# Optimization experiments

Hardware: AMD Instinct MI355X
Metric: run time of the kernel (lower is better)

Reference implementation:

```python
import jax, jax.numpy as jnp
import numpy as np

# --- configuration constants (from OpticalDotProductConfiguration) ---
INPUT_BITS = 8
ADC_BITS = 8
DAC_VMIN, DAC_VMAX = 0.0, 1.0
ADC_VMAX = 1.0
OPT_GAIN = 10.0
AWG_XTALK = 0.01
MZM_VMIN, MZM_VMAX = 0.0, 1.0
MZM_LOSS = 10.0 ** (-0.5 / 10.0)   # loss_dB_to_linear(0.5)
YB_LOSS = 10.0 ** (-0.3 / 10.0)
MRR_LOSS = 10.0 ** (-0.5 / 10.0)
MRR_XTALK = 0.01
PD_RESP = 1.0
PD_DARK = 1e-12
PD_R = 50.0
PD_HZ = 10.0 * 1e9
PD_T = 300.0
TIA_GAIN = 100.0
K_B = 1.380649e-23
Q_E = 1.602176634e-19

B, N = 4096, 8192


def conv_same(x, kernel):
    # x: [B, N], kernel: [K]; torch F.conv1d = cross-correlation, same as lax conv
    out = jax.lax.conv_general_dilated(
        x[:, None, :], kernel[None, None, :], (1,), 'SAME')
    return out[:, 0, :]


def setup_inputs() -> dict:
    key = jax.random.key(0)
    ks = jax.random.split(key, 6)
    return {
        'x': jax.random.normal(ks[0], (B, N), dtype=jnp.float32),
        'weights': jax.random.normal(ks[1], (N,), dtype=jnp.float32),
        'noise_tp': jax.random.normal(ks[2], (B,), dtype=jnp.float32),
        'noise_sp': jax.random.normal(ks[3], (B,), dtype=jnp.float32),
        'noise_tn': jax.random.normal(ks[4], (B,), dtype=jnp.float32),
        'noise_sn': jax.random.normal(ks[5], (B,), dtype=jnp.float32),
    }


def reference(x, weights, noise_tp, noise_sp, noise_tn, noise_sn):
    dt = x.dtype
    # software_implemented_transformation
    wnorm = jnp.max(jnp.abs(weights))
    wnorm = jnp.where(wnorm <= 1e-9, jnp.asarray(1.0, dt), wnorm)
    wt = weights / wnorm
    w_abs = jnp.abs(wt)            # weight DAC is identity for weights
    w_pos = wt >= 0                # [N] bool

    t_pos = x > 0                  # [B, N]
    ax = jnp.abs(x)
    inorm = jnp.max(ax, axis=1)
    inorm = jnp.where(inorm <= 1e-9, jnp.asarray(1.0, dt), inorm)[:, None]
    maxq_in = 2 ** INPUT_BITS - 1
    q = jnp.round(ax / inorm * maxq_in)

    # input DAC
    d = jnp.round(jnp.clip(q, 0.0, maxq_in)) / maxq_in
    d = DAC_VMIN + (DAC_VMAX - DAC_VMIN) * d

    # laser: gain + AWG crosstalk conv
    lk = jnp.array([AWG_XTALK / 4, AWG_XTALK, 1.0, AWG_XTALK, AWG_XTALK / 4], dtype=dt)
    l = conv_same(d * OPT_GAIN, lk)

    # MZM
    m = l * w_abs / (MZM_VMAX - MZM_VMIN) * (YB_LOSS * MZM_LOSS)

    # MRR: masked split, crosstalk conv, loss, reduce over N
    pm = jnp.logical_not(jnp.logical_xor(w_pos[None, :], t_pos)).astype(dt)
    mk = jnp.array([MRR_XTALK / 4, MRR_XTALK, 1.0, MRR_XTALK, MRR_XTALK / 4], dtype=dt)
    pos_sum = jnp.sum(conv_same(m * pm, mk) * MRR_LOSS, axis=1)        # [B]
    neg_sum = jnp.sum(conv_same(m * (1.0 - pm), mk) * MRR_LOSS, axis=1)

    # photodiode with injected noise
    thermal_c = 4.0 * K_B * PD_T * PD_HZ / PD_R
    shot_c = 2.0 * Q_E * PD_HZ

    def pd(t, nth, nsh):
        t = t * PD_RESP + PD_DARK
        t = t + nth * thermal_c
        return t * (1.0 + nsh * shot_c)

    cur = pd(pos_sum, noise_tp, noise_sp) - pd(neg_sum, noise_tn, noise_sn)

    # TIA
    v = jnp.abs(cur * TIA_GAIN)
    sign = (cur >= 0).astype(dt) * 2.0 - 1.0

    # ADC
    sf = (2 ** ADC_BITS - 1) / ADC_VMAX
    va = jnp.round(jnp.clip(v, 0.0, ADC_VMAX) * sf) / sf
    out = va * sign

    scale = wnorm / (2.0 ** (ADC_BITS - INPUT_BITS))
    scale = scale / (OPT_GAIN * TIA_GAIN * MRR_LOSS * YB_LOSS * MZM_LOSS)
    scale = scale / ((PD_RESP + PD_RESP) / 2.0)
    out = out * (scale * inorm[:, 0])
    return out
```

## Files before the change

kernel.cpp:

```cpp
#include <hip/hip_runtime.h>
#include <math.h>

#define NCOL 8192
#define BT   512
#define EPT  16
#define FPT  4

#define MZM_LOSS_D 0.8912509381337456
#define YB_LOSS_D  0.9332543007969910
#define MRR_LOSS_D 0.8912509381337456

__global__ __launch_bounds__(BT, 4)
void odp_main(const float* __restrict__ x, const float* __restrict__ w,
              const float* __restrict__ ntp, const float* __restrict__ nsp,
              const float* __restrict__ ntn, const float* __restrict__ nsn,
              float* __restrict__ out)
{
    __shared__ float  halo[BT][5];
    __shared__ float  redf[16];
    __shared__ double redd[16];
    __shared__ double corrd[4];

    const int t    = threadIdx.x;
    const int lane = t & 63;
    const int wid  = t >> 6;
    const int b    = blockIdx.x;

    const float v_ntp = ntp[b], v_nsp = nsp[b], v_ntn = ntn[b], v_nsn = nsn[b];

    const float4* __restrict__ xr4 = (const float4*)(x + (size_t)b * NCOL);
    const float4* __restrict__ w4  = (const float4*)w;

    float xf[EPT], wf[EPT];
    float mx = 0.f, mw = 0.f;
#pragma unroll
    for (int j = 0; j < FPT; ++j) {
        const float4 xv = xr4[t * FPT + j];
        const float4 wv = w4 [t * FPT + j];
        xf[4*j+0] = xv.x; xf[4*j+1] = xv.y; xf[4*j+2] = xv.z; xf[4*j+3] = xv.w;
        wf[4*j+0] = wv.x; wf[4*j+1] = wv.y; wf[4*j+2] = wv.z; wf[4*j+3] = wv.w;
        mx = fmaxf(mx, fmaxf(fmaxf(fabsf(xv.x), fabsf(xv.y)),
                             fmaxf(fabsf(xv.z), fabsf(xv.w))));
        mw = fmaxf(mw, fmaxf(fmaxf(fabsf(wv.x), fabsf(wv.y)),
                             fmaxf(fabsf(wv.z), fabsf(wv.w))));
    }
#pragma unroll
    for (int off = 32; off; off >>= 1) {
        mx = fmaxf(mx, __shfl_down(mx, off));
        mw = fmaxf(mw, __shfl_down(mw, off));
    }
    if (lane == 0) { redf[wid] = mx; redf[8 + wid] = mw; }
    __syncthreads();

    float inorm = redf[0], wnorm = redf[8];
#pragma unroll
    for (int i = 1; i < 8; ++i) {
        inorm = fmaxf(inorm, redf[i]);
        wnorm = fmaxf(wnorm, redf[8 + i]);
    }
    inorm = (inorm <= 1e-9f) ? 1.f : inorm;
    wnorm = (wnorm <= 1e-9f) ? 1.f : wnorm;

    const double inv_d = 1.0 / (double)inorm;
    const float  y     = (float)inv_d;

    float q[EPT];
#pragma unroll
    for (int c = 0; c < EPT; ++c) {
        const float a  = fabsf(xf[c]);
        const float q0 = a * y;
        const float r  = fmaf(-inorm, q0, a);
        const float t1 = fmaf(r, y, q0);
        q[c] = rintf(t1 * 255.f);
    }
    halo[t][0] = q[0]; halo[t][1] = q[1]; halo[t][2] = q[14]; halo[t][3] = q[15];
    __syncthreads();

    float Q[EPT + 4];
    Q[0] = (t > 0)      ? halo[t - 1][2] : 0.f;
    Q[1] = (t > 0)      ? halo[t - 1][3] : 0.f;
    Q[EPT + 2] = (t < BT - 1) ? halo[t + 1][0] : 0.f;
    Q[EPT + 3] = (t < BT - 1) ? halo[t + 1][1] : 0.f;
#pragma unroll
    for (int c = 0; c < EPT; ++c) Q[c + 2] = q[c];

    const double DE0 = -((double)0.01f + (double)0.0025f);
    const double DE1 = -((double)0.0025f);
    double accP = 0.0, accT = 0.0, cP = 0.0, cT = 0.0;

#pragma unroll
    for (int c = 0; c < EPT; ++c) {
        const float s1   = Q[c + 1] + Q[c + 3];
        const float s2   = Q[c]     + Q[c + 4];
        float conv = fmaf(0.01f, s1, Q[c + 2]);
        conv = fmaf(0.0025f, s2, conv);
        const float u = conv * fabsf(wf[c]);
        const bool  g = (xf[c] > 0.f) == (wf[c] >= 0.f);
        const double ud = (double)u;
        accT += ud;
        accP += g ? ud : 0.0;
        if ((t == 0 && c < 2) || (t == BT - 1 && c >= EPT - 2)) {
            const double de = (c == 0 || c == EPT - 1) ? DE0 : DE1;
            const double du = de * ud;
            cT += du;
            if (g) cP += du;
        }
    }

#pragma unroll
    for (int off = 32; off; off >>= 1) {
        accP += __shfl_down(accP, off);
        accT += __shfl_down(accT, off);
    }
    if (lane == 0)   { redd[wid] = accP; redd[8 + wid] = accT; }
    if (t == 0)      { corrd[0] = cP; corrd[1] = cT; }
    if (t == BT - 1) { corrd[2] = cP; corrd[3] = cT; }
    __syncthreads();

    if (t == 0) {
        double P = 0.0, T = 0.0;
#pragma unroll
        for (int i = 0; i < 8; ++i) { P += redd[i]; T += redd[8 + i]; }
        const double cPs = corrd[0] + corrd[2];
        const double cTs = corrd[1] + corrd[3];

        const double E_MID = 1.0 + 2.0 * (double)0.01f + 2.0 * (double)0.0025f;
        const double Kd = (10.0 / 255.0) * (YB_LOSS_D * MZM_LOSS_D) / (double)wnorm;

        const double ps = (P * E_MID + cPs) * Kd * MRR_LOSS_D;
        const double ns = ((T - P) * E_MID + (cTs - cPs)) * Kd * MRR_LOSS_D;

        const float thermal_f = 3.3135576e-12f;
        const float shot_f    = 3.204353268e-9f;

        double tp_ = ps + 1e-12 + (double)(v_ntp * thermal_f);
        tp_ *= (double)(1.0f + v_nsp * shot_f);
        double tn_ = ns + 1e-12 + (double)(v_ntn * thermal_f);
        tn_ *= (double)(1.0f + v_nsn * shot_f);

        const double cur = tp_ - tn_;
        double v = fabs(cur * 100.0);
        v = fmin(v, 1.0);
        const double va  = rint(v * 255.0) * (1.0 / 255.0);
        const double sgn = (cur >= 0.0) ? 1.0 : -1.0;
        const double scale = (double)wnorm /
            (10.0 * 100.0 * MRR_LOSS_D * YB_LOSS_D * MZM_LOSS_D);
        out[b] = (float)(va * sgn * scale * (double)inorm);
    }
}

extern "C" void kernel_launch(void* const* d_in, const int* in_sizes, int n_in,
                              void* d_out, int out_size, void* d_ws, size_t ws_size,
                              hipStream_t stream) {
    const float* x   = (const float*)d_in[0];
    const float* w   = (const float*)d_in[1];
    const float* ntp = (const float*)d_in[2];
    const float* nsp = (const float*)d_in[3];
    const float* ntn = (const float*)d_in[4];
    const float* nsn = (const float*)d_in[5];
    float* out = (float*)d_out;
    odp_main<<<dim3(out_size), dim3(BT), 0, stream>>>(x, w, ntp, nsp, ntn, nsn, out);
}
```

Baseline: 33.39 us.

## Load halo from global, accumulate signed/total sums in float

Each thread now reads its two neighbouring elements directly from global memory and quantizes them itself, which removes the shared-memory halo exchange and one block barrier. The positive/negative split is rewritten algebraically as a signed sum D and a total T (pos=(T+D)/2, neg=(T-D)/2). These are accumulated in float across four partial accumulators, and conversion to double happens only at the per-thread and warp level. This cuts per-element double-precision work and branching. The risk is lower accumulation precision and cancellation in (T-D), which could flip ADC rounding results.

```diff
diff --git a/kernel.cpp b/kernel.cpp
--- a/kernel.cpp
+++ b/kernel.cpp
@@ -4,7 +4,6 @@
 #define NCOL 8192
 #define BT   512
 #define EPT  16
-#define FPT  4
 
 #define MZM_LOSS_D 0.8912509381337456
 #define YB_LOSS_D  0.9332543007969910
@@ -16,9 +15,9 @@
               const float* __restrict__ ntn, const float* __restrict__ nsn,
               float* __restrict__ out)
 {
-    __shared__ float  halo[BT][5];
     __shared__ float  redf[16];
-    __shared__ double redd[16];
+    __shared__ float  redT[8];
+    __shared__ double redD[8];
     __shared__ double corrd[4];
 
     const int t    = threadIdx.x;
@@ -28,17 +27,23 @@
 
     const float v_ntp = ntp[b], v_nsp = nsp[b], v_ntn = ntn[b], v_nsn = nsn[b];
 
-    const float4* __restrict__ xr4 = (const float4*)(x + (size_t)b * NCOL);
-    const float4* __restrict__ w4  = (const float4*)w;
+    const float*  __restrict__ xrow = x + (size_t)b * NCOL;
+    const float4* __restrict__ xr4  = (const float4*)xrow;
+    const float4* __restrict__ w4   = (const float4*)w;
 
     float xf[EPT], wf[EPT];
+    const int hL = (t > 0)      ? (t * EPT - 2)   : 0;
+    const int hR = (t < BT - 1) ? (t * EPT + EPT) : (NCOL - 2);
+    const float2 hxL = *(const float2*)(xrow + hL);
+    const float2 hxR = *(const float2*)(xrow + hR);
+
     float mx = 0.f, mw = 0.f;
 #pragma unroll
-    for (int j = 0; j < FPT; ++j) {
-        const float4 xv = xr4[t * FPT + j];
-        const float4 wv = w4 [t * FPT + j];
-        xf[4*j+0] = xv.x; xf[4*j+1] = xv.y; xf[4*j+2] = xv.z; xf[4*j+3] = xv.w;
-        wf[4*j+0] = wv.x; wf[4*j+1] = wv.y; wf[4*j+2] = wv.z; wf[4*j+3] = wv.w;
+    for (int j = 0; j < 4; ++j) {
+        const float4 xv = xr4[t * 4 + j];
+        const float4 wv = w4 [t * 4 + j];
+        xf[4*j+0]=xv.x; xf[4*j+1]=xv.y; xf[4*j+2]=xv.z; xf[4*j+3]=xv.w;
+        wf[4*j+0]=wv.x; wf[4*j+1]=wv.y; wf[4*j+2]=wv.z; wf[4*j+3]=wv.w;
         mx = fmaxf(mx, fmaxf(fmaxf(fabsf(xv.x), fabsf(xv.y)),
                              fmaxf(fabsf(xv.z), fabsf(xv.w))));
         mw = fmaxf(mw, fmaxf(fmaxf(fabsf(wv.x), fabsf(wv.y)),
@@ -64,71 +69,76 @@
     const double inv_d = 1.0 / (double)inorm;
     const float  y     = (float)inv_d;
 
-    float q[EPT];
+    float Q[EPT + 4];
 #pragma unroll
     for (int c = 0; c < EPT; ++c) {
         const float a  = fabsf(xf[c]);
         const float q0 = a * y;
         const float r  = fmaf(-inorm, q0, a);
-        const float t1 = fmaf(r, y, q0);
-        q[c] = rintf(t1 * 255.f);
+        Q[c + 2] = rintf(fmaf(r, y, q0) * 255.f);
     }
-    halo[t][0] = q[0]; halo[t][1] = q[1]; halo[t][2] = q[14]; halo[t][3] = q[15];
-    __syncthreads();
+    {
+        const float aL0 = fabsf(hxL.x), aL1 = fabsf(hxL.y);
+        const float aR0 = fabsf(hxR.x), aR1 = fabsf(hxR.y);
+        float q0, r;
+        q0 = aL0 * y; r = fmaf(-inorm, q0, aL0); Q[0]  = rintf(fmaf(r, y, q0) * 255.f);
+        q0 = aL1 * y; r = fmaf(-inorm, q0, aL1); Q[1]  = rintf(fmaf(r, y, q0) * 255.f);
+        q0 = aR0 * y; r = fmaf(-inorm, q0, aR0); Q[18] = rintf(fmaf(r, y, q0) * 255.f);
+        q0 = aR1 * y; r = fmaf(-inorm, q0, aR1); Q[19] = rintf(fmaf(r, y, q0) * 255.f);
+        if (t == 0)      { Q[0]  = 0.f; Q[1]  = 0.f; }
+        if (t == BT - 1) { Q[18] = 0.f; Q[19] = 0.f; }
+    }
 
-    float Q[EPT + 4];
-    Q[0] = (t > 0)      ? halo[t - 1][2] : 0.f;
-    Q[1] = (t > 0)      ? halo[t - 1][3] : 0.f;
-    Q[EPT + 2] = (t < BT - 1) ? halo[t + 1][0] : 0.f;
-    Q[EPT + 3] = (t < BT - 1) ? halo[t + 1][1] : 0.f;
-#pragma unroll
-    for (int c = 0; c < EPT; ++c) Q[c + 2] = q[c];
-
+    float Dv[4] = {0.f,0.f,0.f,0.f}, Tv[4] = {0.f,0.f,0.f,0.f};
+    double cD = 0.0, cT = 0.0;
     const double DE0 = -((double)0.01f + (double)0.0025f);
     const double DE1 = -((double)0.0025f);
-    double accP = 0.0, accT = 0.0, cP = 0.0, cT = 0.0;
 
 #pragma unroll
     for (int c = 0; c < EPT; ++c) {
-        const float s1   = Q[c + 1] + Q[c + 3];
-        const float s2   = Q[c]     + Q[c + 4];
+        const float s1 = Q[c + 1] + Q[c + 3];
+        const float s2 = Q[c]     + Q[c + 4];
         float conv = fmaf(0.01f, s1, Q[c + 2]);
         conv = fmaf(0.0025f, s2, conv);
-        const float u = conv * fabsf(wf[c]);
-        const bool  g = (xf[c] > 0.f) == (wf[c] >= 0.f);
-        const double ud = (double)u;
-        accT += ud;
-        accP += g ? ud : 0.0;
-        if ((t == 0 && c < 2) || (t == BT - 1 && c >= EPT - 2)) {
-            const double de = (c == 0 || c == EPT - 1) ? DE0 : DE1;
-            const double du = de * ud;
-            cT += du;
-            if (g) cP += du;
+        const float sel = (xf[c] > 0.f) ? wf[c] : -wf[c];
+        Dv[c & 3] = fmaf(conv, sel,        Dv[c & 3]);
+        Tv[c & 3] = fmaf(conv, fabsf(sel), Tv[c & 3]);
+        if (t == 0 && c < 2) {
+            const double de = (c == 0) ? DE0 : DE1;
+            cD += de * (double)(conv * sel);
+            cT += de * (double)(conv * fabsf(sel));
+        }
+        if (t == BT - 1 && c >= EPT - 2) {
+            const double de = (c == EPT - 1) ? DE0 : DE1;
+            cD += de * (double)(conv * sel);
+            cT += de * (double)(conv * fabsf(sel));
         }
     }
 
+    double accD = ((double)Dv[0] + (double)Dv[1]) + ((double)Dv[2] + (double)Dv[3]);
+    float  accT = (Tv[0] + Tv[1]) + (Tv[2] + Tv[3]);
+
 #pragma unroll
     for (int off = 32; off; off >>= 1) {
-        accP += __shfl_down(accP, off);
+        accD += __shfl_down(accD, off);
         accT += __shfl_down(accT, off);
     }
-    if (lane == 0)   { redd[wid] = accP; redd[8 + wid] = accT; }
-    if (t == 0)      { corrd[0] = cP; corrd[1] = cT; }
-    if (t == BT - 1) { corrd[2] = cP; corrd[3] = cT; }
+    if (lane == 0)   { redD[wid] = accD; redT[wid] = accT; }
+    if (t == 0)      { corrd[0] = cD; corrd[1] = cT; }
+    if (t == BT - 1) { corrd[2] = cD; corrd[3] = cT; }
     __syncthreads();
 
     if (t == 0) {
-        double P = 0.0, T = 0.0;
+        double D = 0.0, T = 0.0;
 #pragma unroll
-        for (int i = 0; i < 8; ++i) { P += redd[i]; T += redd[8 + i]; }
-        const double cPs = corrd[0] + corrd[2];
-        const double cTs = corrd[1] + corrd[3];
+        for (int i = 0; i < 8; ++i) { D += redD[i]; T += (double)redT[i]; }
+        const double E_MID = 1.0 + 2.0 * (double)0.01f + 2.0 * (double)0.0025f;
+        D = D * E_MID + (corrd[0] + corrd[2]);
+        T = T * E_MID + (corrd[1] + corrd[3]);
 
-        const double E_MID = 1.0 + 2.0 * (double)0.01f + 2.0 * (double)0.0025f;
         const double Kd = (10.0 / 255.0) * (YB_LOSS_D * MZM_LOSS_D) / (double)wnorm;
-
-        const double ps = (P * E_MID + cPs) * Kd * MRR_LOSS_D;
-        const double ns = ((T - P) * E_MID + (cTs - cPs)) * Kd * MRR_LOSS_D;
+        const double ps = (T + D) * 0.5 * Kd * MRR_LOSS_D;
+        const double ns = (T - D) * 0.5 * Kd * MRR_LOSS_D;
 
         const float thermal_f = 3.3135576e-12f;
         const float shot_f    = 3.204353268e-9f;
```

Result: faster. 30.31 us (-9.2%).

## Process eight rows per block with double-buffered row prefetch and halo loads

Applied to the files above, without the earlier changes.

Each block now handles eight rows instead of one, loading and reducing the weight vector once and reusing it across rows. The next row's data is prefetched into registers while the current row is processed. Neighbour halos are read directly from global memory instead of through a shared-memory exchange, which removes one barrier per row. The positive/negative split is rewritten as signed and total float accumulations, so the per-element double adds are gone. Exchanges: grid drops to 512 blocks, which may underfill the GPU, register pressure rises, and float accumulation may change rounding near ADC thresholds.

```diff
diff --git a/kernel.cpp b/kernel.cpp
--- a/kernel.cpp
+++ b/kernel.cpp
@@ -4,11 +4,146 @@
 #define NCOL 8192
 #define BT   512
 #define EPT  16
-#define FPT  4
+#define ROWS 8
 
 #define MZM_LOSS_D 0.8912509381337456
 #define YB_LOSS_D  0.9332543007969910
 #define MRR_LOSS_D 0.8912509381337456
+
+#define LOADX(XV, HL, HR, ROWIDX) do {                                        \
+    const float* xr_ = x + (size_t)(ROWIDX) * NCOL;                           \
+    const float4* xr4_ = (const float4*)xr_;                                  \
+    _Pragma("unroll")                                                         \
+    for (int j = 0; j < 4; ++j) {                                             \
+        const float4 xv_ = xr4_[t * 4 + j];                                   \
+        XV[4*j+0]=xv_.x; XV[4*j+1]=xv_.y; XV[4*j+2]=xv_.z; XV[4*j+3]=xv_.w;   \
+    }                                                                         \
+    HL = *(const float2*)(xr_ + ((t > 0)      ? (t*EPT - 2)   : 0));          \
+    HR = *(const float2*)(xr_ + ((t < BT - 1) ? (t*EPT + EPT) : (NCOL - 2))); \
+} while (0)
+
+#define ROW_BODY(R, XC, HLC, HRC, PREFETCH) do {                              \
+    const int row_ = r0 + (R);                                                \
+    const float vntp_ = ntp[row_], vnsp_ = nsp[row_];                         \
+    const float vntn_ = ntn[row_], vnsn_ = nsn[row_];                         \
+    PREFETCH;                                                                 \
+    float mx_ = 0.f;                                                          \
+    _Pragma("unroll")                                                         \
+    for (int c = 0; c < EPT; ++c) mx_ = fmaxf(mx_, fabsf(XC[c]));             \
+    _Pragma("unroll")                                                         \
+    for (int off = 32; off; off >>= 1) mx_ = fmaxf(mx_, __shfl_down(mx_, off));\
+    if (lane == 0) redX[R][wid] = mx_;                                        \
+    if ((R) == 0 && lane == 0) redW[wid] = mw;                                \
+    asm volatile("s_waitcnt lgkmcnt(0)" ::: "memory");                        \
+    __builtin_amdgcn_s_barrier();                                             \
+    float inorm_ = redX[R][0];                                                \
+    _Pragma("unroll")                                                         \
+    for (int i = 1; i < 8; ++i) inorm_ = fmaxf(inorm_, redX[R][i]);           \
+    inorm_ = (inorm_ <= 1e-9f) ? 1.f : inorm_;                                \
+    if ((R) == 0) {                                                           \
+        float wn_ = redW[0];                                                  \
+        _Pragma("unroll")                                                     \
+        for (int i = 1; i < 8; ++i) wn_ = fmaxf(wn_, redW[i]);                \
+        wnorm = (wn_ <= 1e-9f) ? 1.f : wn_;                                   \
+    }                                                                         \
+    const double invd_ = 1.0 / (double)inorm_;                                \
+    const float  y_    = (float)invd_;                                        \
+    float Q[EPT + 4];                                                         \
+    _Pragma("unroll")                                                         \
+    for (int c = 0; c < EPT; ++c) {                                           \
+        const float a_  = fabsf(XC[c]);                                       \
+        const float q0_ = a_ * y_;                                            \
+        const float r_  = fmaf(-inorm_, q0_, a_);                             \
+        Q[c + 2] = rintf(fmaf(r_, y_, q0_) * 255.f);                          \
+    }                                                                         \
+    {                                                                         \
+        const float aL0_=fabsf(HLC.x), aL1_=fabsf(HLC.y);                     \
+        const float aR0_=fabsf(HRC.x), aR1_=fabsf(HRC.y);                     \
+        float q0_, r_;                                                        \
+        q0_=aL0_*y_; r_=fmaf(-inorm_,q0_,aL0_); Q[0] =rintf(fmaf(r_,y_,q0_)*255.f);\
+        q0_=aL1_*y_; r_=fmaf(-inorm_,q0_,aL1_); Q[1] =rintf(fmaf(r_,y_,q0_)*255.f);\
+        q0_=aR0_*y_; r_=fmaf(-inorm_,q0_,aR0_); Q[18]=rintf(fmaf(r_,y_,q0_)*255.f);\
+        q0_=aR1_*y_; r_=fmaf(-inorm_,q0_,aR1_); Q[19]=rintf(fmaf(r_,y_,q0_)*255.f);\
+        if (t == 0)      { Q[0]  = 0.f; Q[1]  = 0.f; }                        \
+        if (t == BT - 1) { Q[18] = 0.f; Q[19] = 0.f; }                        \
+    }                                                                         \
+    float Dv_[4] = {0.f,0.f,0.f,0.f}, Tv_[4] = {0.f,0.f,0.f,0.f};             \
+    double cD_ = 0.0, cT_ = 0.0;                                              \
+    _Pragma("unroll")                                                         \
+    for (int c = 0; c < EPT; ++c) {                                           \
+        const float s1_ = Q[c + 1] + Q[c + 3];                                \
+        const float s2_ = Q[c]     + Q[c + 4];                                \
+        float cv_ = fmaf(0.01f, s1_, Q[c + 2]);                               \
+        cv_ = fmaf(0.0025f, s2_, cv_);                                        \
+        const float sel_ = (XC[c] > 0.f) ? wf[c] : -wf[c];                    \
+        Dv_[c & 3] = fmaf(cv_, sel_,        Dv_[c & 3]);                      \
+        Tv_[c & 3] = fmaf(cv_, fabsf(sel_), Tv_[c & 3]);                      \
+    }                                                                         \
+    if (t == 0) {                                                             \
+        _Pragma("unroll")                                                     \
+        for (int c = 0; c < 2; ++c) {                                         \
+            const float s1_ = Q[c + 1] + Q[c + 3];                            \
+            const float s2_ = Q[c]     + Q[c + 4];                            \
+            float cv_ = fmaf(0.01f, s1_, Q[c + 2]);                           \
+            cv_ = fmaf(0.0025f, s2_, cv_);                                    \
+            const float sel_ = (XC[c] > 0.f) ? wf[c] : -wf[c];                \
+            const double de_ = (c == 0) ? DE0 : DE1;                          \
+            cD_ += de_ * (double)(cv_ * sel_);                                \
+            cT_ += de_ * (double)(cv_ * fabsf(sel_));                         \
+        }                                                                     \
+    }                                                                         \
+    if (t == BT - 1) {                                                        \
+        _Pragma("unroll")                                                     \
+        for (int c = EPT - 2; c < EPT; ++c) {                                 \
+            const float s1_ = Q[c + 1] + Q[c + 3];                            \
+            const float s2_ = Q[c]     + Q[c + 4];                            \
+            float cv_ = fmaf(0.01f, s1_, Q[c + 2]);                           \
+            cv_ = fmaf(0.0025f, s2_, cv_);                                    \
+            const float sel_ = (XC[c] > 0.f) ? wf[c] : -wf[c];                \
+            const double de_ = (c == EPT - 1) ? DE0 : DE1;                    \
+            cD_ += de_ * (double)(cv_ * sel_);                                \
+            cT_ += de_ * (double)(cv_ * fabsf(sel_));                         \
+        }                                                                     \
+    }                                                                         \
+    double accD_ = ((double)Dv_[0] + (double)Dv_[1])                          \
+                 + ((double)Dv_[2] + (double)Dv_[3]);                         \
+    float  accT_ = (Tv_[0] + Tv_[1]) + (Tv_[2] + Tv_[3]);                     \
+    _Pragma("unroll")                                                         \
+    for (int off = 32; off; off >>= 1) {                                      \
+        accD_ += __shfl_down(accD_, off);                                     \
+        accT_ += __shfl_down(accT_, off);                                     \
+    }                                                                         \
+    if (lane == 0)   { redD[R][wid] = accD_; redT[R][wid] = accT_; }          \
+    if (t == 0)      { corrd[R][0] = cD_; corrd[R][1] = cT_; }                \
+    if (t == BT - 1) { corrd[R][2] = cD_; corrd[R][3] = cT_; }                \
+    asm volatile("s_waitcnt lgkmcnt(0)" ::: "memory");                        \
+    __builtin_amdgcn_s_barrier();                                             \
+    if (t == 0) {                                                             \
+        double D_ = 0.0, T_ = 0.0;                                            \
+        _Pragma("unroll")                                                     \
+        for (int i = 0; i < 8; ++i) { D_ += redD[R][i]; T_ += (double)redT[R][i]; } \
+        const double E_MID = 1.0 + 2.0 * (double)0.01f + 2.0 * (double)0.0025f;\
+        D_ = D_ * E_MID + (corrd[R][0] + corrd[R][2]);                        \
+        T_ = T_ * E_MID + (corrd[R][1] + corrd[R][3]);                        \
+        const double Kd = (10.0 / 255.0) * (YB_LOSS_D * MZM_LOSS_D) / (double)wnorm;\
+        const double ps = (T_ + D_) * 0.5 * Kd * MRR_LOSS_D;                  \
+        const double ns = (T_ - D_) * 0.5 * Kd * MRR_LOSS_D;                  \
+        const float thermal_f = 3.3135576e-12f;                               \
+        const float shot_f    = 3.204353268e-9f;                              \
+        double tp_ = ps + 1e-12 + (double)(vntp_ * thermal_f);                \
+        tp_ *= (double)(1.0f + vnsp_ * shot_f);                               \
+        double tn_ = ns + 1e-12 + (double)(vntn_ * thermal_f);                \
+        tn_ *= (double)(1.0f + vnsn_ * shot_f);                               \
+        const double cur = tp_ - tn_;                                         \
+        double v_ = fabs(cur * 100.0);                                        \
+        v_ = fmin(v_, 1.0);                                                   \
+        const double va_  = rint(v_ * 255.0) * (1.0 / 255.0);                 \
+        const double sgn_ = (cur >= 0.0) ? 1.0 : -1.0;                        \
+        const double scale_ = (double)wnorm /                                 \
+            (10.0 * 100.0 * MRR_LOSS_D * YB_LOSS_D * MZM_LOSS_D);             \
+        out[row_] = (float)(va_ * sgn_ * scale_ * (double)inorm_);            \
+    }                                                                         \
+} while (0)
 
 __global__ __launch_bounds__(BT, 4)
 void odp_main(const float* __restrict__ x, const float* __restrict__ w,
@@ -16,137 +151,48 @@
               const float* __restrict__ ntn, const float* __restrict__ nsn,
               float* __restrict__ out)
 {
-    __shared__ float  halo[BT][5];
-    __shared__ float  redf[16];
-    __shared__ double redd[16];
-    __shared__ double corrd[4];
+    __shared__ float  redX[ROWS][8];
+    __shared__ float  redW[8];
+    __shared__ float  redT[ROWS][8];
+    __shared__ double redD[ROWS][8];
+    __shared__ double corrd[ROWS][4];
 
     const int t    = threadIdx.x;
     const int lane = t & 63;
     const int wid  = t >> 6;
-    const int b    = blockIdx.x;
-
-    const float v_ntp = ntp[b], v_nsp = nsp[b], v_ntn = ntn[b], v_nsn = nsn[b];
-
-    const float4* __restrict__ xr4 = (const float4*)(x + (size_t)b * NCOL);
-    const float4* __restrict__ w4  = (const float4*)w;
-
-    float xf[EPT], wf[EPT];
-    float mx = 0.f, mw = 0.f;
+    const int r0   = blockIdx.x * ROWS;
+
+    const double DE0 = -((double)0.01f + (double)0.0025f);
+    const double DE1 = -((double)0.0025f);
+
+    const float4* __restrict__ w4 = (const float4*)w;
+    float wf[EPT];
+    float mw = 0.f;
 #pragma unroll
-    for (int j = 0; j < FPT; ++j) {
-        const float4 xv = xr4[t * FPT + j];
-        const float4 wv = w4 [t * FPT + j];
-        xf[4*j+0] = xv.x; xf[4*j+1] = xv.y; xf[4*j+2] = xv.z; xf[4*j+3] = xv.w;
-        wf[4*j+0] = wv.x; wf[4*j+1] = wv.y; wf[4*j+2] = wv.z; wf[4*j+3] = wv.w;
-        mx = fmaxf(mx, fmaxf(fmaxf(fabsf(xv.x), fabsf(xv.y)),
-                             fmaxf(fabsf(xv.z), fabsf(xv.w))));
+    for (int j = 0; j < 4; ++j) {
+        const float4 wv = w4[t * 4 + j];
+        wf[4*j+0]=wv.x; wf[4*j+1]=wv.y; wf[4*j+2]=wv.z; wf[4*j+3]=wv.w;
         mw = fmaxf(mw, fmaxf(fmaxf(fabsf(wv.x), fabsf(wv.y)),
                              fmaxf(fabsf(wv.z), fabsf(wv.w))));
     }
 #pragma unroll
-    for (int off = 32; off; off >>= 1) {
-        mx = fmaxf(mx, __shfl_down(mx, off));
+    for (int off = 32; off; off >>= 1)
         mw = fmaxf(mw, __shfl_down(mw, off));
-    }
-    if (lane == 0) { redf[wid] = mx; redf[8 + wid] = mw; }
-    __syncthreads();
-
-    float inorm = redf[0], wnorm = redf[8];
-#pragma unroll
-    for (int i = 1; i < 8; ++i) {
-        inorm = fmaxf(inorm, redf[i]);
-        wnorm = fmaxf(wnorm, redf[8 + i]);
-    }
-    inorm = (inorm <= 1e-9f) ? 1.f : inorm;
-    wnorm = (wnorm <= 1e-9f) ? 1.f : wnorm;
-
-    const double inv_d = 1.0 / (double)inorm;
-    const float  y     = (float)inv_d;
-
-    float q[EPT];
-#pragma unroll
-    for (int c = 0; c < EPT; ++c) {
-        const float a  = fabsf(xf[c]);
-        const float q0 = a * y;
-        const float r  = fmaf(-inorm, q0, a);
-        const float t1 = fmaf(r, y, q0);
-        q[c] = rintf(t1 * 255.f);
-    }
-    halo[t][0] = q[0]; halo[t][1] = q[1]; halo[t][2] = q[14]; halo[t][3] = q[15];
-    __syncthreads();
-
-    float Q[EPT + 4];
-    Q[0] = (t > 0)      ? halo[t - 1][2] : 0.f;
-    Q[1] = (t > 0)      ? halo[t - 1][3] : 0.f;
-    Q[EPT + 2] = (t < BT - 1) ? halo[t + 1][0] : 0.f;
-    Q[EPT + 3] = (t < BT - 1) ? halo[t + 1][1] : 0.f;
-#pragma unroll
-    for (int c = 0; c < EPT; ++c) Q[c + 2] = q[c];
-
-    const double DE0 = -((double)0.01f + (double)0.0025f);
-    const double DE1 = -((double)0.0025f);
-    double accP = 0.0, accT = 0.0, cP = 0.0, cT = 0.0;
-
-#pragma unroll
-    for (int c = 0; c < EPT; ++c) {
-        const float s1   = Q[c + 1] + Q[c + 3];
-        const float s2   = Q[c]     + Q[c + 4];
-        float conv = fmaf(0.01f, s1, Q[c + 2]);
-        conv = fmaf(0.0025f, s2, conv);
-        const float u = conv * fabsf(wf[c]);
-        const bool  g = (xf[c] > 0.f) == (wf[c] >= 0.f);
-        const double ud = (double)u;
-        accT += ud;
-        accP += g ? ud : 0.0;
-        if ((t == 0 && c < 2) || (t == BT - 1 && c >= EPT - 2)) {
-            const double de = (c == 0 || c == EPT - 1) ? DE0 : DE1;
-            const double du = de * ud;
-            cT += du;
-            if (g) cP += du;
-        }
-    }
-
-#pragma unroll
-    for (int off = 32; off; off >>= 1) {
-        accP += __shfl_down(accP, off);
-        accT += __shfl_down(accT, off);
-    }
-    if (lane == 0)   { redd[wid] = accP; redd[8 + wid] = accT; }
-    if (t == 0)      { corrd[0] = cP; corrd[1] = cT; }
-    if (t == BT - 1) { corrd[2] = cP; corrd[3] = cT; }
-    __syncthreads();
-
-    if (t == 0) {
-        double P = 0.0, T = 0.0;
-#pragma unroll
-        for (int i = 0; i < 8; ++i) { P += redd[i]; T += redd[8 + i]; }
-        const double cPs = corrd[0] + corrd[2];
-        const double cTs = corrd[1] + corrd[3];
-
-        const double E_MID = 1.0 + 2.0 * (double)0.01f + 2.0 * (double)0.0025f;
-        const double Kd = (10.0 / 255.0) * (YB_LOSS_D * MZM_LOSS_D) / (double)wnorm;
-
-        const double ps = (P * E_MID + cPs) * Kd * MRR_LOSS_D;
-        const double ns = ((T - P) * E_MID + (cTs - cPs)) * Kd * MRR_LOSS_D;
-
-        const float thermal_f = 3.3135576e-12f;
-        const float shot_f    = 3.204353268e-9f;
-
-        double tp_ = ps + 1e-12 + (double)(v_ntp * thermal_f);
-        tp_ *= (double)(1.0f + v_nsp * shot_f);
-        double tn_ = ns + 1e-12 + (double)(v_ntn * thermal_f);
-        tn_ *= (double)(1.0f + v_nsn * shot_f);
-
-        const double cur = tp_ - tn_;
-        double v = fabs(cur * 100.0);
-        v = fmin(v, 1.0);
-        const double va  = rint(v * 255.0) * (1.0 / 255.0);
-        const double sgn = (cur >= 0.0) ? 1.0 : -1.0;
-        const double scale = (double)wnorm /
-            (10.0 * 100.0 * MRR_LOSS_D * YB_LOSS_D * MZM_LOSS_D);
-        out[b] = (float)(va * sgn * scale * (double)inorm);
-    }
+
+    float xA[EPT], xB[EPT];
+    float2 hLA, hRA, hLB, hRB;
+    LOADX(xA, hLA, hRA, r0);
+
+    float wnorm = 1.f;
+
+    ROW_BODY(0, xA, hLA, hRA, LOADX(xB, hLB, hRB, r0 + 1));
+    ROW_BODY(1, xB, hLB, hRB, LOADX(xA, hLA, hRA, r0 + 2));
+    ROW_BODY(2, xA, hLA, hRA, LOADX(xB, hLB, hRB, r0 + 3));
+    ROW_BODY(3, xB, hLB, hRB, LOADX(xA, hLA, hRA, r0 + 4));
+    ROW_BODY(4, xA, hLA, hRA, LOADX(xB, hLB, hRB, r0 + 5));
+    ROW_BODY(5, xB, hLB, hRB, LOADX(xA, hLA, hRA, r0 + 6));
+    ROW_BODY(6, xA, hLA, hRA, LOADX(xB, hLB, hRB, r0 + 7));
+    ROW_BODY(7, xB, hLB, hRB, ((void)0));
 }
 
 extern "C" void kernel_launch(void* const* d_in, const int* in_sizes, int n_in,
@@ -159,5 +205,6 @@
     const float* ntn = (const float*)d_in[4];
     const float* nsn = (const float*)d_in[5];
     float* out = (float*)d_out;
-    odp_main<<<dim3(out_size), dim3(BT), 0, stream>>>(x, w, ntp, nsp, ntn, nsn, out);
+    const int nblocks = (out_size + ROWS - 1) / ROWS;
+    odp_main<<<dim3(nblocks), dim3(BT), 0, stream>>>(x, w, ntp, nsp, ntn, nsn, out);
 }
```

New measurement: 32.34 us. 1.03x faster.

## Process two rows per block, load halos from global, interleave reductions

Applied to the files above, without the earlier changes.

Each block now handles two rows, which halves the grid and reuses the weight vector load and its max reduction across both rows. The shared-memory halo exchange is replaced by direct float2 global loads of neighbour elements, with quantisation recomputed per thread. Accumulation moves from double to float with four partial sums, and the signed difference D replaces the masked P sum. The second row's reduction overlaps the first row's tail. In exchange, register pressure rises and float accumulation may change rounding of the sums.

```diff
diff --git a/kernel.cpp b/kernel.cpp
--- a/kernel.cpp
+++ b/kernel.cpp
@@ -4,11 +4,78 @@
 #define NCOL 8192
 #define BT   512
 #define EPT  16
-#define FPT  4
+#define ROWS 2
 
 #define MZM_LOSS_D 0.8912509381337456
 #define YB_LOSS_D  0.9332543007969910
 #define MRR_LOSS_D 0.8912509381337456
+
+static __device__ __forceinline__ void lds_barrier() {
+    asm volatile("s_waitcnt lgkmcnt(0)" ::: "memory");
+    __builtin_amdgcn_s_barrier();
+}
+
+#define QF(dst, a_, INORM, Y) do {                         \
+    const float a__  = (a_);                               \
+    const float q0__ = a__ * (Y);                          \
+    const float r__  = fmaf(-(INORM), q0__, a__);          \
+    (dst) = rintf(fmaf(r__, (Y), q0__) * 255.f);           \
+} while (0)
+
+#define ROW_COMPUTE(XF, HXL, HXR, INORM, Y, ACCD, ACCT, CDV, CTV) do {        \
+    float Q[EPT + 4];                                                         \
+    _Pragma("unroll")                                                         \
+    for (int c = 0; c < EPT; ++c) QF(Q[c + 2], fabsf(XF[c]), INORM, Y);       \
+    QF(Q[0],  fabsf(HXL.x), INORM, Y);                                        \
+    QF(Q[1],  fabsf(HXL.y), INORM, Y);                                        \
+    QF(Q[18], fabsf(HXR.x), INORM, Y);                                        \
+    QF(Q[19], fabsf(HXR.y), INORM, Y);                                        \
+    if (t == 0)      { Q[0]  = 0.f; Q[1]  = 0.f; }                            \
+    if (t == BT - 1) { Q[18] = 0.f; Q[19] = 0.f; }                            \
+    float Dv[4] = {0.f,0.f,0.f,0.f}, Tv[4] = {0.f,0.f,0.f,0.f};               \
+    _Pragma("unroll")                                                         \
+    for (int c = 0; c < EPT; ++c) {                                           \
+        const float s1 = Q[c + 1] + Q[c + 3];                                 \
+        const float s2 = Q[c]     + Q[c + 4];                                 \
+        float cv = fmaf(0.01f, s1, Q[c + 2]);                                 \
+        cv = fmaf(0.0025f, s2, cv);                                           \
+        const float sel = (XF[c] > 0.f) ? wf[c] : -wf[c];                     \
+        Dv[c & 3] = fmaf(cv, sel,        Dv[c & 3]);                          \
+        Tv[c & 3] = fmaf(cv, fabsf(sel), Tv[c & 3]);                          \
+        if ((t == 0 && c < 2) || (t == BT - 1 && c >= EPT - 2)) {             \
+            const double de = (c == 0 || c == EPT - 1) ? DE0 : DE1;           \
+            CDV += de * (double)(cv * sel);                                   \
+            CTV += de * (double)(cv * fabsf(sel));                            \
+        }                                                                     \
+    }                                                                         \
+    ACCD = ((double)Dv[0] + (double)Dv[1]) + ((double)Dv[2] + (double)Dv[3]); \
+    ACCT = (Tv[0] + Tv[1]) + (Tv[2] + Tv[3]);                                 \
+} while (0)
+
+#define ROW_TAIL(REDD, REDT, CORR, INORM, NTP, NSP, NTN, NSN, OV) do {        \
+    double D = 0.0, T = 0.0;                                                  \
+    _Pragma("unroll")                                                         \
+    for (int i = 0; i < 8; ++i) { D += REDD[i]; T += (double)REDT[i]; }       \
+    D = D * E_MID + (CORR[0] + CORR[2]);                                      \
+    T = T * E_MID + (CORR[1] + CORR[3]);                                      \
+    const double Kd = (10.0 / 255.0) * (YB_LOSS_D * MZM_LOSS_D) / (double)wnorm;\
+    const double ps = (T + D) * 0.5 * Kd * MRR_LOSS_D;                        \
+    const double ns = (T - D) * 0.5 * Kd * MRR_LOSS_D;                        \
+    const float thermal_f = 3.3135576e-12f;                                   \
+    const float shot_f    = 3.204353268e-9f;                                  \
+    double tp_ = ps + 1e-12 + (double)((NTP) * thermal_f);                    \
+    tp_ *= (double)(1.0f + (NSP) * shot_f);                                   \
+    double tn_ = ns + 1e-12 + (double)((NTN) * thermal_f);                    \
+    tn_ *= (double)(1.0f + (NSN) * shot_f);                                   \
+    const double cur = tp_ - tn_;                                             \
+    double v = fabs(cur * 100.0);                                             \
+    v = fmin(v, 1.0);                                                         \
+    const double va  = rint(v * 255.0) * (1.0 / 255.0);                       \
+    const double sgn = (cur >= 0.0) ? 1.0 : -1.0;                             \
+    const double scale = (double)wnorm /                                      \
+        (10.0 * 100.0 * MRR_LOSS_D * YB_LOSS_D * MZM_LOSS_D);                 \
+    OV = (float)(va * sgn * scale * (double)(INORM));                         \
+} while (0)
 
 __global__ __launch_bounds__(BT, 4)
 void odp_main(const float* __restrict__ x, const float* __restrict__ w,
@@ -16,136 +83,127 @@
               const float* __restrict__ ntn, const float* __restrict__ nsn,
               float* __restrict__ out)
 {
-    __shared__ float  halo[BT][5];
-    __shared__ float  redf[16];
-    __shared__ double redd[16];
-    __shared__ double corrd[4];
+    __shared__ float  redX0[8], redX1[8], redW[8];
+    __shared__ float  redT0[8], redT1[8];
+    __shared__ double redD0[8], redD1[8];
+    __shared__ double corr0[4], corr1[4];
 
     const int t    = threadIdx.x;
     const int lane = t & 63;
     const int wid  = t >> 6;
-    const int b    = blockIdx.x;
-
-    const float v_ntp = ntp[b], v_nsp = nsp[b], v_ntn = ntn[b], v_nsn = nsn[b];
-
-    const float4* __restrict__ xr4 = (const float4*)(x + (size_t)b * NCOL);
-    const float4* __restrict__ w4  = (const float4*)w;
-
-    float xf[EPT], wf[EPT];
-    float mx = 0.f, mw = 0.f;
-#pragma unroll
-    for (int j = 0; j < FPT; ++j) {
-        const float4 xv = xr4[t * FPT + j];
-        const float4 wv = w4 [t * FPT + j];
-        xf[4*j+0] = xv.x; xf[4*j+1] = xv.y; xf[4*j+2] = xv.z; xf[4*j+3] = xv.w;
-        wf[4*j+0] = wv.x; wf[4*j+1] = wv.y; wf[4*j+2] = wv.z; wf[4*j+3] = wv.w;
-        mx = fmaxf(mx, fmaxf(fmaxf(fabsf(xv.x), fabsf(xv.y)),
-                             fmaxf(fabsf(xv.z), fabsf(xv.w))));
-        mw = fmaxf(mw, fmaxf(fmaxf(fabsf(wv.x), fabsf(wv.y)),
-                             fmaxf(fabsf(wv.z), fabsf(wv.w))));
-    }
-#pragma unroll
-    for (int off = 32; off; off >>= 1) {
-        mx = fmaxf(mx, __shfl_down(mx, off));
-        mw = fmaxf(mw, __shfl_down(mw, off));
-    }
-    if (lane == 0) { redf[wid] = mx; redf[8 + wid] = mw; }
-    __syncthreads();
-
-    float inorm = redf[0], wnorm = redf[8];
-#pragma unroll
-    for (int i = 1; i < 8; ++i) {
-        inorm = fmaxf(inorm, redf[i]);
-        wnorm = fmaxf(wnorm, redf[8 + i]);
-    }
-    inorm = (inorm <= 1e-9f) ? 1.f : inorm;
-    wnorm = (wnorm <= 1e-9f) ? 1.f : wnorm;
-
-    const double inv_d = 1.0 / (double)inorm;
-    const float  y     = (float)inv_d;
-
-    float q[EPT];
-#pragma unroll
-    for (int c = 0; c < EPT; ++c) {
-        const float a  = fabsf(xf[c]);
-        const float q0 = a * y;
-        const float r  = fmaf(-inorm, q0, a);
-        const float t1 = fmaf(r, y, q0);
-        q[c] = rintf(t1 * 255.f);
-    }
-    halo[t][0] = q[0]; halo[t][1] = q[1]; halo[t][2] = q[14]; halo[t][3] = q[15];
-    __syncthreads();
-
-    float Q[EPT + 4];
-    Q[0] = (t > 0)      ? halo[t - 1][2] : 0.f;
-    Q[1] = (t > 0)      ? halo[t - 1][3] : 0.f;
-    Q[EPT + 2] = (t < BT - 1) ? halo[t + 1][0] : 0.f;
-    Q[EPT + 3] = (t < BT - 1) ? halo[t + 1][1] : 0.f;
-#pragma unroll
-    for (int c = 0; c < EPT; ++c) Q[c + 2] = q[c];
+    const int r0   = blockIdx.x * ROWS;
 
     const double DE0 = -((double)0.01f + (double)0.0025f);
     const double DE1 = -((double)0.0025f);
-    double accP = 0.0, accT = 0.0, cP = 0.0, cT = 0.0;
-
-#pragma unroll
-    for (int c = 0; c < EPT; ++c) {
-        const float s1   = Q[c + 1] + Q[c + 3];
-        const float s2   = Q[c]     + Q[c + 4];
-        float conv = fmaf(0.01f, s1, Q[c + 2]);
-        conv = fmaf(0.0025f, s2, conv);
-        const float u = conv * fabsf(wf[c]);
-        const bool  g = (xf[c] > 0.f) == (wf[c] >= 0.f);
-        const double ud = (double)u;
-        accT += ud;
-        accP += g ? ud : 0.0;
-        if ((t == 0 && c < 2) || (t == BT - 1 && c >= EPT - 2)) {
-            const double de = (c == 0 || c == EPT - 1) ? DE0 : DE1;
-            const double du = de * ud;
-            cT += du;
-            if (g) cP += du;
-        }
-    }
+    const double E_MID = 1.0 + 2.0 * (double)0.01f + 2.0 * (double)0.0025f;
+
+    const float vntp0 = ntp[r0],     vnsp0 = nsp[r0];
+    const float vntn0 = ntn[r0],     vnsn0 = nsn[r0];
+    const float vntp1 = ntp[r0 + 1], vnsp1 = nsp[r0 + 1];
+    const float vntn1 = ntn[r0 + 1], vnsn1 = nsn[r0 + 1];
+
+    const float*  __restrict__ xrow0 = x + (size_t)r0 * NCOL;
+    const float*  __restrict__ xrow1 = xrow0 + NCOL;
+    const float4* __restrict__ xr40  = (const float4*)xrow0;
+    const float4* __restrict__ xr41  = (const float4*)xrow1;
+    const float4* __restrict__ w4    = (const float4*)w;
+
+    float xf0[EPT], xf1[EPT], wf[EPT];
+#pragma unroll
+    for (int j = 0; j < 4; ++j) {
+        const float4 v = xr40[t * 4 + j];
+        xf0[4*j+0]=v.x; xf0[4*j+1]=v.y; xf0[4*j+2]=v.z; xf0[4*j+3]=v.w;
+    }
+    const float2 hxL0 = *(const float2*)(xrow0 + ((t > 0)      ? t*EPT - 2   : 0));
+    const float2 hxR0 = *(const float2*)(xrow0 + ((t < BT - 1) ? t*EPT + EPT : NCOL - 2));
+#pragma unroll
+    for (int j = 0; j < 4; ++j) {
+        const float4 v = w4[t * 4 + j];
+        wf[4*j+0]=v.x; wf[4*j+1]=v.y; wf[4*j+2]=v.z; wf[4*j+3]=v.w;
+    }
+#pragma unroll
+    for (int j = 0; j < 4; ++j) {
+        const float4 v = xr41[t * 4 + j];
+        xf1[4*j+0]=v.x; xf1[4*j+1]=v.y; xf1[4*j+2]=v.z; xf1[4*j+3]=v.w;
+    }
+    const float2 hxL1 = *(const float2*)(xrow1 + ((t > 0)      ? t*EPT - 2   : 0));
+    const float2 hxR1 = *(const float2*)(xrow1 + ((t < BT - 1) ? t*EPT + EPT : NCOL - 2));
+
+    float mx0 = 0.f;
+#pragma unroll
+    for (int c = 0; c < EPT; ++c) mx0 = fmaxf(mx0, fabsf(xf0[c]));
+#pragma unroll
+    for (int off = 32; off; off >>= 1)
+        mx0 = fmaxf(mx0, __shfl_down(mx0, off));
+    if (lane == 0) redX0[wid] = mx0;
+    lds_barrier();
+
+    float inorm0 = redX0[0];
+#pragma unroll
+    for (int i = 1; i < 8; ++i) inorm0 = fmaxf(inorm0, redX0[i]);
+    inorm0 = (inorm0 <= 1e-9f) ? 1.f : inorm0;
+    const double invd0 = 1.0 / (double)inorm0;
+    const float  y0    = (float)invd0;
+
+    float mw = 0.f;
+#pragma unroll
+    for (int c = 0; c < EPT; ++c) mw = fmaxf(mw, fabsf(wf[c]));
+
+    double accD0, cD0 = 0.0, cT0 = 0.0;
+    float  accT0;
+    ROW_COMPUTE(xf0, hxL0, hxR0, inorm0, y0, accD0, accT0, cD0, cT0);
+
+    float mx1 = 0.f;
+#pragma unroll
+    for (int c = 0; c < EPT; ++c) mx1 = fmaxf(mx1, fabsf(xf1[c]));
+#pragma unroll
+    for (int off = 32; off; off >>= 1)
+        mx1 = fmaxf(mx1, __shfl_down(mx1, off));
+    if (lane == 0) redX1[wid] = mx1;
 
 #pragma unroll
     for (int off = 32; off; off >>= 1) {
-        accP += __shfl_down(accP, off);
-        accT += __shfl_down(accT, off);
-    }
-    if (lane == 0)   { redd[wid] = accP; redd[8 + wid] = accT; }
-    if (t == 0)      { corrd[0] = cP; corrd[1] = cT; }
-    if (t == BT - 1) { corrd[2] = cP; corrd[3] = cT; }
-    __syncthreads();
+        accD0 += __shfl_down(accD0, off);
+        accT0 += __shfl_down(accT0, off);
+        mw     = fmaxf(mw, __shfl_down(mw, off));
+    }
+    if (lane == 0)   { redD0[wid] = accD0; redT0[wid] = accT0; redW[wid] = mw; }
+    if (t == 0)      { corr0[0] = cD0; corr0[1] = cT0; }
+    if (t == BT - 1) { corr0[2] = cD0; corr0[3] = cT0; }
+    lds_barrier();
+
+    float wnorm = redW[0];
+#pragma unroll
+    for (int i = 1; i < 8; ++i) wnorm = fmaxf(wnorm, redW[i]);
+    wnorm = (wnorm <= 1e-9f) ? 1.f : wnorm;
+
+    float ov0 = 0.f, ov1 = 0.f;
+    if (t == 0) ROW_TAIL(redD0, redT0, corr0, inorm0, vntp0, vnsp0, vntn0, vnsn0, ov0);
+
+    float inorm1 = redX1[0];
+#pragma unroll
+    for (int i = 1; i < 8; ++i) inorm1 = fmaxf(inorm1, redX1[i]);
+    inorm1 = (inorm1 <= 1e-9f) ? 1.f : inorm1;
+    const double invd1 = 1.0 / (double)inorm1;
+    const float  y1    = (float)invd1;
+
+    double accD1, cD1 = 0.0, cT1 = 0.0;
+    float  accT1;
+    ROW_COMPUTE(xf1, hxL1, hxR1, inorm1, y1, accD1, accT1, cD1, cT1);
+
+#pragma unroll
+    for (int off = 32; off; off >>= 1) {
+        accD1 += __shfl_down(accD1, off);
+        accT1 += __shfl_down(accT1, off);
+    }
+    if (lane == 0)   { redD1[wid] = accD1; redT1[wid] = accT1; }
+    if (t == 0)      { corr1[0] = cD1; corr1[1] = cT1; }
+    if (t == BT - 1) { corr1[2] = cD1; corr1[3] = cT1; }
+    lds_barrier();
 
     if (t == 0) {
-        double P = 0.0, T = 0.0;
-#pragma unroll
-        for (int i = 0; i < 8; ++i) { P += redd[i]; T += redd[8 + i]; }
-        const double cPs = corrd[0] + corrd[2];
-        const double cTs = corrd[1] + corrd[3];
-
-        const double E_MID = 1.0 + 2.0 * (double)0.01f + 2.0 * (double)0.0025f;
-        const double Kd = (10.0 / 255.0) * (YB_LOSS_D * MZM_LOSS_D) / (double)wnorm;
-
-        const double ps = (P * E_MID + cPs) * Kd * MRR_LOSS_D;
-        const double ns = ((T - P) * E_MID + (cTs - cPs)) * Kd * MRR_LOSS_D;
-
-        const float thermal_f = 3.3135576e-12f;
-        const float shot_f    = 3.204353268e-9f;
-
-        double tp_ = ps + 1e-12 + (double)(v_ntp * thermal_f);
-        tp_ *= (double)(1.0f + v_nsp * shot_f);
-        double tn_ = ns + 1e-12 + (double)(v_ntn * thermal_f);
-        tn_ *= (double)(1.0f + v_nsn * shot_f);
-
-        const double cur = tp_ - tn_;
-        double v = fabs(cur * 100.0);
-        v = fmin(v, 1.0);
-        const double va  = rint(v * 255.0) * (1.0 / 255.0);
-        const double sgn = (cur >= 0.0) ? 1.0 : -1.0;
-        const double scale = (double)wnorm /
-            (10.0 * 100.0 * MRR_LOSS_D * YB_LOSS_D * MZM_LOSS_D);
-        out[b] = (float)(va * sgn * scale * (double)inorm);
+        ROW_TAIL(redD1, redT1, corr1, inorm1, vntp1, vnsp1, vntn1, vnsn1, ov1);
+        *(float2*)(out + r0) = make_float2(ov0, ov1);
     }
 }
 
@@ -159,5 +217,6 @@
     const float* ntn = (const float*)d_in[4];
     const float* nsn = (const float*)d_in[5];
     float* out = (float*)d_out;
-    odp_main<<<dim3(out_size), dim3(BT), 0, stream>>>(x, w, ntp, nsp, ntn, nsn, out);
+    const int nblocks = out_size / ROWS;
+    odp_main<<<dim3(nblocks), dim3(BT), 0, stream>>>(x, w, ntp, nsp, ntn, nsn, out);
 }
```

After: 31.34 us. -6.1%, faster.
